# Kernel tuning notes

Hardware: AMD Instinct MI355X
Metric: run time of the kernel (lower is better)

The kernel has to match this reference:

```python
import math
import jax, jax.numpy as jnp
import numpy as np


def setup_inputs() -> dict:
    key = jax.random.key(0)
    k1, k2 = jax.random.split(key)
    N, C, K = 1024, 4096, 16384
    x = jax.random.normal(k1, (N, C), dtype=jnp.float32)
    # xavier_normal for (C, K): std = sqrt(2/(C+K))
    w_std = math.sqrt(2.0 / (C + K))
    weights = jax.random.normal(k2, (C, K), dtype=jnp.float32) * w_std
    std = jnp.float32(10.0)
    return {"x": x, "weights": weights, "std": std}


def reference(x, weights, std):
    # x: (N, C); weights: (C, K)
    N, C = x.shape
    K = weights.shape[1]
    side = int(math.sqrt(K))

    # Squared distances ||w_k - x_n||^2 via expansion (same math as
    # norm(weights[None] - x[..., None], dim=1)**2, without the (N,C,K) tensor)
    x2 = jnp.sum(x * x, axis=1, keepdims=True)            # (N, 1)
    w2 = jnp.sum(weights * weights, axis=0)[None, :]       # (1, K)
    xw = jnp.einsum('nc,ck->nk', x, weights)               # (N, K) GEMM
    norms2 = jnp.maximum(x2 + w2 - 2.0 * xw, 0.0)          # (N, K)

    # Best matching unit (detached in original)
    bmu = jnp.argmin(norms2, axis=-1)                      # (N,) int

    # 2D radial basis over the side x side grid, centered at BMU
    row = (bmu // side).astype(jnp.float32)
    col = (bmu % side).astype(jnp.float32)
    t = jnp.arange(side, dtype=jnp.float32)
    gi, gj = jnp.meshgrid(t, t, indexing='ij')
    grid = jnp.stack([gi.reshape(-1), gj.reshape(-1)], axis=-1)  # (K, 2)
    pt = jnp.stack([row, col], axis=-1)[:, None, :]              # (N, 1, 2)
    d2 = jnp.sum((grid[None] - pt) ** 2, axis=-1)                # (N, K)
    phi = jnp.exp(-0.5 * d2 / (std ** 2))
    phi = phi / jnp.sum(phi, axis=-1, keepdims=True)

    return norms2 * phi
```

## Files before the change

### kernel.cpp

```cpp
#include <hip/hip_runtime.h>
#include <stdint.h>

#define NROWS 1024
#define CDIM  4096
#define KDIM  16384
#define SIDE  128

typedef __attribute__((ext_vector_type(8))) short short8;
typedef __attribute__((ext_vector_type(4))) float f32x4;

static __device__ __forceinline__ unsigned short f2bf(float f) {
  unsigned u = __float_as_uint(f);
  u += 0x7fffu + ((u >> 16) & 1u);
  return (unsigned short)(u >> 16);
}
static __device__ __forceinline__ float bf2f(unsigned short h) {
  return __uint_as_float(((unsigned)h) << 16);
}

#define GLOAD_LDS16(g, l)                                                     \
  __builtin_amdgcn_global_load_lds(                                           \
      (const __attribute__((address_space(1))) void*)(g),                     \
      (__attribute__((address_space(3))) void*)(l), 16, 0, 0)

#define SWZ(o) ((o) ^ (((o) >> 3) & 0x70))

__global__ void k_zero(float* __restrict__ w2) {
  w2[blockIdx.x * 256 + threadIdx.x] = 0.f;
}

__global__ __launch_bounds__(256) void k_wconv(const float* __restrict__ w,
                                               unsigned short* __restrict__ whT,
                                               unsigned short* __restrict__ wlT,
                                               float* __restrict__ w2) {
  __shared__ float T[64][65];
  const int k0 = blockIdx.x * 64, c0 = blockIdx.y * 64;
  const int t = threadIdx.x;
#pragma unroll
  for (int i = 0; i < 4; i++) {
    int e = i * 1024 + t * 4;
    int cr = e >> 6, kc = e & 63;
    float4 v = *(const float4*)(w + (size_t)(c0 + cr) * KDIM + k0 + kc);
    T[cr][kc] = v.x; T[cr][kc + 1] = v.y; T[cr][kc + 2] = v.z; T[cr][kc + 3] = v.w;
  }
  __syncthreads();
#pragma unroll
  for (int i = 0; i < 4; i++) {
    int e = i * 1024 + t * 4;
    int kr = e >> 6, cc = e & 63;
    ushort4 hv, lv;
    float f0 = T[cc + 0][kr], f1 = T[cc + 1][kr];
    float f2 = T[cc + 2][kr], f3 = T[cc + 3][kr];
    hv.x = f2bf(f0); lv.x = f2bf(f0 - bf2f(hv.x));
    hv.y = f2bf(f1); lv.y = f2bf(f1 - bf2f(hv.y));
    hv.z = f2bf(f2); lv.z = f2bf(f2 - bf2f(hv.z));
    hv.w = f2bf(f3); lv.w = f2bf(f3 - bf2f(hv.w));
    size_t off = (size_t)(k0 + kr) * CDIM + c0 + cc;
    *(ushort4*)(whT + off) = hv;
    *(ushort4*)(wlT + off) = lv;
    float s = f0 * f0 + f1 * f1 + f2 * f2 + f3 * f3;
#pragma unroll
    for (int off2 = 8; off2 > 0; off2 >>= 1) s += __shfl_down(s, off2);
    if ((t & 15) == 0) atomicAdd(&w2[k0 + kr], s);
  }
}

__global__ __launch_bounds__(256) void k_xconv(const float* __restrict__ x,
                                               unsigned short* __restrict__ xh) {
  size_t i = ((size_t)blockIdx.x * 256 + threadIdx.x) * 4;
  float4 v = *(const float4*)(x + i);
  ushort4 hv;
  hv.x = f2bf(v.x); hv.y = f2bf(v.y); hv.z = f2bf(v.z); hv.w = f2bf(v.w);
  *(ushort4*)(xh + i) = hv;
}

__global__ void k_x2(const float* __restrict__ x, float* __restrict__ x2) {
  const int n = blockIdx.x, l = threadIdx.x;
  const float* row = x + (size_t)n * CDIM;
  float s = 0.f;
#pragma unroll 4
  for (int i = 0; i < 16; i++) {
    float4 v = *(const float4*)(row + (i * 64 + l) * 4);
    s += v.x * v.x + v.y * v.y + v.z * v.z + v.w * v.w;
  }
#pragma unroll
  for (int off = 32; off > 0; off >>= 1) s += __shfl_down(s, off);
  if (l == 0) x2[n] = s;
}

__global__ __launch_bounds__(512, 2) void k_gemm(
    const unsigned short* __restrict__ xh,
    const unsigned short* __restrict__ whT,
    const float* __restrict__ x2, const float* __restrict__ w2,
    float* __restrict__ out) {
  __shared__ alignas(128) char smem[49152];
  char* const Ah = smem;
  char* const Bh = smem + 32768;
  const int t = threadIdx.x;
  const int b = blockIdx.x;
  const int wg = (b & 7) * 64 + (b >> 3);
  const int m0 = (wg & 3) * 256, n0 = (wg >> 2) * 128;
  const int lane = t & 63, wid = t >> 6;
  const int wr = (wid >> 1) * 64;
  const int wc = (wid & 1) * 64;

  int rowA[4], cbA[4];
  uint32_t loffA[4];
#pragma unroll
  for (int i = 0; i < 4; i++) {
    int o_lin = (i * 512 + t) * 16;
    int o_log = SWZ(o_lin);
    rowA[i] = o_log >> 7;
    cbA[i] = (o_log & 127) >> 1;
    loffA[i] = i * 8192 + wid * 1024;
  }
  int rowB[2], cbB[2];
  uint32_t loffB[2];
#pragma unroll
  for (int i = 0; i < 2; i++) {
    int o_lin = (i * 512 + t) * 16;
    int o_log = SWZ(o_lin);
    rowB[i] = o_log >> 7;
    cbB[i] = (o_log & 127) >> 1;
    loffB[i] = i * 8192 + wid * 1024;
  }

  f32x4 acc[4][4];
#pragma unroll
  for (int m = 0; m < 4; m++)
#pragma unroll
    for (int n = 0; n < 4; n++) acc[m][n] = (f32x4){0.f, 0.f, 0.f, 0.f};

  const int rlo = lane & 15;
  const int kgb = (lane >> 4) * 16;

  for (int c0 = 0; c0 < CDIM; c0 += 64) {
#pragma unroll
    for (int i = 0; i < 4; i++) {
      size_t ga = (size_t)(m0 + rowA[i]) * CDIM + c0 + cbA[i];
      GLOAD_LDS16(xh + ga, Ah + loffA[i]);
    }
#pragma unroll
    for (int i = 0; i < 2; i++) {
      size_t gb = (size_t)(n0 + rowB[i]) * CDIM + c0 + cbB[i];
      GLOAD_LDS16(whT + gb, Bh + loffB[i]);
    }
    __syncthreads();

#pragma unroll
    for (int h = 0; h < 2; h++) {
      const int cby = h * 64 + kgb;
      short8 b_f[4];
#pragma unroll
      for (int n = 0; n < 4; n++)
        b_f[n] = *(const short8*)(Bh + SWZ((wc + n * 16 + rlo) * 128 + cby));
#pragma unroll
      for (int m = 0; m < 4; m++) {
        short8 ah = *(const short8*)(Ah + SWZ((wr + m * 16 + rlo) * 128 + cby));
#pragma unroll
        for (int n = 0; n < 4; n++)
          acc[m][n] = __builtin_amdgcn_mfma_f32_16x16x32_bf16(ah, b_f[n], acc[m][n], 0, 0, 0);
      }
    }
    __syncthreads();
  }

  float w2v[4];
#pragma unroll
  for (int n = 0; n < 4; n++) w2v[n] = w2[n0 + wc + n * 16 + rlo];
#pragma unroll
  for (int m = 0; m < 4; m++) {
#pragma unroll
    for (int j = 0; j < 4; j++) {
      int row = m0 + wr + m * 16 + (lane >> 4) * 4 + j;
      float xr = x2[row];
      float* orow = out + (size_t)row * KDIM;
#pragma unroll
      for (int n = 0; n < 4; n++) {
        int col = n0 + wc + n * 16 + rlo;
        float v = xr + w2v[n] - 2.0f * acc[m][n][j];
        orow[col] = v < 0.f ? 0.f : v;
      }
    }
  }
}

__global__ __launch_bounds__(256) void k_fb(const float* __restrict__ x,
                                            const float* __restrict__ w,
                                            float* __restrict__ out) {
  __shared__ float xs[16][65];
  __shared__ float wsm[16][65];
  const int t = threadIdx.x;
  const int n0 = blockIdx.x * 64, k0 = blockIdx.y * 64;
  const int tx = t & 15, ty = t >> 4;
  float acc[4][4];
#pragma unroll
  for (int a = 0; a < 4; a++)
#pragma unroll
    for (int b = 0; b < 4; b++) acc[a][b] = 0.f;
  for (int c0 = 0; c0 < CDIM; c0 += 16) {
#pragma unroll
    for (int i = 0; i < 4; i++) {
      int e = i * 256 + t;
      int nl = e >> 4, cl = e & 15;
      xs[cl][nl] = x[(size_t)(n0 + nl) * CDIM + c0 + cl];
    }
#pragma unroll
    for (int i = 0; i < 4; i++) {
      int e = i * 256 + t;
      int cl = e >> 6, kl = e & 63;
      wsm[cl][kl] = w[(size_t)(c0 + cl) * KDIM + k0 + kl];
    }
    __syncthreads();
#pragma unroll
    for (int c = 0; c < 16; c++)
#pragma unroll
      for (int a = 0; a < 4; a++) {
        float xa = xs[c][ty * 4 + a];
#pragma unroll
        for (int b = 0; b < 4; b++) {
          float d = wsm[c][tx * 4 + b] - xa;
          acc[a][b] += d * d;
        }
      }
    __syncthreads();
  }
#pragma unroll
  for (int a = 0; a < 4; a++)
#pragma unroll
    for (int b = 0; b < 4; b++)
      out[(size_t)(n0 + ty * 4 + a) * KDIM + k0 + tx * 4 + b] = acc[a][b];
}

__global__ __launch_bounds__(256) void k_row(
    float* __restrict__ out, const float* __restrict__ stdp,
    const float* __restrict__ x, const unsigned short* __restrict__ whT,
    const unsigned short* __restrict__ wlT, const float* __restrict__ w2) {
  const int n = blockIdx.x, t = threadIdx.x;
  __shared__ alignas(16) float er[SIDE];
  __shared__ alignas(16) float ec[SIDE];
  __shared__ float rv[4];
  __shared__ float s_red[4];
  __shared__ int cand[128];
  __shared__ int s_ncand;
  __shared__ int s_bmu;
  __shared__ float s_inv;
  float* row = out + (size_t)n * KDIM;

  float bv = 3.4e38f;
#pragma unroll 4
  for (int i = 0; i < 16; i++) {
    float4 v = *(const float4*)(row + (t + i * 256) * 4);
    bv = fminf(fminf(fminf(bv, v.x), fminf(v.y, v.z)), v.w);
  }
#pragma unroll
  for (int off = 32; off > 0; off >>= 1) bv = fminf(bv, __shfl_down(bv, off));
  if ((t & 63) == 0) rv[t >> 6] = bv;
  if (t == 0) s_ncand = 0;
  __syncthreads();
  const float thr = fminf(fminf(rv[0], rv[1]), fminf(rv[2], rv[3])) + 0.05f;

#pragma unroll 4
  for (int i = 0; i < 16; i++) {
    int k = (t + i * 256) * 4;
    float4 v = *(const float4*)(row + k);
    if (v.x <= thr) { int j = atomicAdd(&s_ncand, 1); if (j < 128) cand[j] = k; }
    if (v.y <= thr) { int j = atomicAdd(&s_ncand, 1); if (j < 128) cand[j] = k + 1; }
    if (v.z <= thr) { int j = atomicAdd(&s_ncand, 1); if (j < 128) cand[j] = k + 2; }
    if (v.w <= thr) { int j = atomicAdd(&s_ncand, 1); if (j < 128) cand[j] = k + 3; }
  }
  __syncthreads();
  int nc = s_ncand < 128 ? s_ncand : 128;

  float best = 3.4e38f;
  int bestk = 0x7fffffff;
  const float* xr = x + (size_t)n * CDIM;
  for (int j = 0; j < nc; j++) {
    const int k = cand[j];
    const unsigned short* wh = whT + (size_t)k * CDIM;
    const unsigned short* wl = wlT + (size_t)k * CDIM;
    float s = 0.f;
#pragma unroll
    for (int ii = 0; ii < 2; ii++) {
      int c = (ii * 256 + t) * 8;
      short8 h8 = *(const short8*)(wh + c);
      short8 l8 = *(const short8*)(wl + c);
      float4 xa = *(const float4*)(xr + c);
      float4 xb = *(const float4*)(xr + c + 4);
      s += xa.x * (bf2f((unsigned short)h8[0]) + bf2f((unsigned short)l8[0]));
      s += xa.y * (bf2f((unsigned short)h8[1]) + bf2f((unsigned short)l8[1]));
      s += xa.z * (bf2f((unsigned short)h8[2]) + bf2f((unsigned short)l8[2]));
      s += xa.w * (bf2f((unsigned short)h8[3]) + bf2f((unsigned short)l8[3]));
      s += xb.x * (bf2f((unsigned short)h8[4]) + bf2f((unsigned short)l8[4]));
      s += xb.y * (bf2f((unsigned short)h8[5]) + bf2f((unsigned short)l8[5]));
      s += xb.z * (bf2f((unsigned short)h8[6]) + bf2f((unsigned short)l8[6]));
      s += xb.w * (bf2f((unsigned short)h8[7]) + bf2f((unsigned short)l8[7]));
    }
#pragma unroll
    for (int off = 32; off > 0; off >>= 1) s += __shfl_down(s, off);
    if ((t & 63) == 0) s_red[t >> 6] = s;
    __syncthreads();
    if (t == 0) {
      float dot = s_red[0] + s_red[1] + s_red[2] + s_red[3];
      float sc = w2[k] - 2.0f * dot;
      if (sc < best || (sc == best && k < bestk)) { best = sc; bestk = k; }
    }
    __syncthreads();
  }
  if (t == 0) s_bmu = bestk;
  __syncthreads();

  const int bmu = s_bmu;
  const float sd = stdp[0];
  const float inv2s2 = -0.5f / (sd * sd);
  const float rr = (float)(bmu >> 7), ccol = (float)(bmu & 127);
  if (t < 128) {
    float d = (float)t - rr;
    er[t] = expf(d * d * inv2s2);
  } else {
    int j = t - 128;
    float d = (float)j - ccol;
    ec[j] = expf(d * d * inv2s2);
  }
  __syncthreads();
  if (t == 0) {
    float Sr = 0.f, Sc = 0.f;
    for (int i = 0; i < SIDE; i++) { Sr += er[i]; Sc += ec[i]; }
    s_inv = 1.0f / (Sr * Sc);
  }
  __syncthreads();
  const float inv = s_inv;
#pragma unroll 4
  for (int i = 0; i < 16; i++) {
    int k = (t + i * 256) * 4;
    float4 v = *(const float4*)(row + k);
    float e_r = er[k >> 7] * inv;
    const float4 e4 = *(const float4*)(&ec[k & 127]);
    v.x *= e_r * e4.x;
    v.y *= e_r * e4.y;
    v.z *= e_r * e4.z;
    v.w *= e_r * e4.w;
    *(float4*)(row + k) = v;
  }
}

__global__ __launch_bounds__(256) void k_row_fb(float* __restrict__ out,
                                                const float* __restrict__ stdp) {
  const int n = blockIdx.x, t = threadIdx.x;
  __shared__ alignas(16) float er[SIDE];
  __shared__ alignas(16) float ec[SIDE];
  __shared__ float rv[4];
  __shared__ int ri[4];
  __shared__ float s_inv;
  __shared__ int s_bmu;
  float* row = out + (size_t)n * KDIM;

  float bv = 3.4e38f;
  int bi = 0;
#pragma unroll 4
  for (int i = 0; i < 16; i++) {
    int k = (t + i * 256) * 4;
    float4 v = *(const float4*)(row + k);
    if (v.x < bv) { bv = v.x; bi = k; }
    if (v.y < bv) { bv = v.y; bi = k + 1; }
    if (v.z < bv) { bv = v.z; bi = k + 2; }
    if (v.w < bv) { bv = v.w; bi = k + 3; }
  }
#pragma unroll
  for (int off = 32; off > 0; off >>= 1) {
    float ov = __shfl_down(bv, off);
    int oi = __shfl_down(bi, off);
    if (ov < bv || (ov == bv && oi < bi)) { bv = ov; bi = oi; }
  }
  if ((t & 63) == 0) { rv[t >> 6] = bv; ri[t >> 6] = bi; }
  __syncthreads();
  if (t == 0) {
    for (int i = 1; i < 4; i++)
      if (rv[i] < bv || (rv[i] == bv && ri[i] < bi)) { bv = rv[i]; bi = ri[i]; }
    s_bmu = bi;
  }
  __syncthreads();
  const int bmu = s_bmu;
  const float sd = stdp[0];
  const float inv2s2 = -0.5f / (sd * sd);
  const float rr = (float)(bmu >> 7), ccol = (float)(bmu & 127);
  if (t < 128) {
    float d = (float)t - rr;
    er[t] = expf(d * d * inv2s2);
  } else {
    int j = t - 128;
    float d = (float)j - ccol;
    ec[j] = expf(d * d * inv2s2);
  }
  __syncthreads();
  if (t == 0) {
    float Sr = 0.f, Sc = 0.f;
    for (int i = 0; i < SIDE; i++) { Sr += er[i]; Sc += ec[i]; }
    s_inv = 1.0f / (Sr * Sc);
  }
  __syncthreads();
  const float inv = s_inv;
#pragma unroll 4
  for (int i = 0; i < 16; i++) {
    int k = (t + i * 256) * 4;
    float4 v = *(const float4*)(row + k);
    float e_r = er[k >> 7] * inv;
    const float4 e4 = *(const float4*)(&ec[k & 127]);
    v.x *= e_r * e4.x;
    v.y *= e_r * e4.y;
    v.z *= e_r * e4.z;
    v.w *= e_r * e4.w;
    *(float4*)(row + k) = v;
  }
}

extern "C" void kernel_launch(void* const* d_in, const int* in_sizes, int n_in,
                              void* d_out, int out_size, void* d_ws, size_t ws_size,
                              hipStream_t stream) {
  (void)in_sizes; (void)n_in; (void)out_size;
  const float* x = (const float*)d_in[0];
  const float* w = (const float*)d_in[1];
  const float* stdp = (const float*)d_in[2];
  float* out = (float*)d_out;

  const size_t sz_wT = (size_t)KDIM * CDIM * sizeof(unsigned short);
  const size_t sz_x  = (size_t)NROWS * CDIM * sizeof(unsigned short);
  const size_t need = 2 * sz_wT + sz_x + (size_t)NROWS * 4 + (size_t)KDIM * 4;

  if (ws_size >= need) {
    char* p = (char*)d_ws;
    unsigned short* whT = (unsigned short*)p; p += sz_wT;
    unsigned short* wlT = (unsigned short*)p; p += sz_wT;
    unsigned short* xh  = (unsigned short*)p; p += sz_x;
    float* x2 = (float*)p; p += (size_t)NROWS * 4;
    float* w2 = (float*)p;

    k_zero<<<KDIM / 256, 256, 0, stream>>>(w2);
    k_wconv<<<dim3(KDIM / 64, CDIM / 64), 256, 0, stream>>>(w, whT, wlT, w2);
    k_xconv<<<(NROWS * CDIM) / 1024, 256, 0, stream>>>(x, xh);
    k_x2<<<NROWS, 64, 0, stream>>>(x, x2);
    k_gemm<<<512, 512, 0, stream>>>(xh, whT, x2, w2, out);
    k_row<<<NROWS, 256, 0, stream>>>(out, stdp, x, whT, wlT, w2);
  } else {
    k_fb<<<dim3(NROWS / 64, KDIM / 64), 256, 0, stream>>>(x, w, out);
    k_row_fb<<<NROWS, 256, 0, stream>>>(out, stdp);
  }
}
```

Measured before the change: 307.8 us.

## Double-buffer GEMM LDS tiles and enlarge block tile to 256x256

The bf16 GEMM kernel moves to a 256x256 output tile per workgroup, with each wave computing 128x64, and halves the grid to 256 blocks. The next K-tile is loaded into a second 64KB LDS buffer while the current one is computed, using explicit vmcnt waits and raw barriers in place of the blocking load-then-sync loop. MFMA sections are given raised wave priority. It needs 128KB of dynamic LDS, which gives one block per CU and doubles the accumulator registers. With only 256 blocks the grid may underfill the GPU's CUs.

New measurement: 293.2 us. 1.05x faster.

```diff
diff --git a/kernel.cpp b/kernel.cpp
--- a/kernel.cpp
+++ b/kernel.cpp
@@ -93,91 +93,102 @@
     const unsigned short* __restrict__ whT,
     const float* __restrict__ x2, const float* __restrict__ w2,
     float* __restrict__ out) {
-  __shared__ alignas(128) char smem[49152];
-  char* const Ah = smem;
-  char* const Bh = smem + 32768;
+  extern __shared__ char smem[];
   const int t = threadIdx.x;
   const int b = blockIdx.x;
-  const int wg = (b & 7) * 64 + (b >> 3);
-  const int m0 = (wg & 3) * 256, n0 = (wg >> 2) * 128;
+  const int L = (b & 7) * 32 + (b >> 3);
+  const int m0 = (L & 3) * 256, n0 = (L >> 2) * 256;
   const int lane = t & 63, wid = t >> 6;
-  const int wr = (wid >> 1) * 64;
-  const int wc = (wid & 1) * 64;
-
-  int rowA[4], cbA[4];
-  uint32_t loffA[4];
+  const int wrow = (wid >> 2) * 128;
+  const int wcol = (wid & 3) * 64;
+
+  int rowS[4], cbS[4];
+  uint32_t loffS[4];
 #pragma unroll
   for (int i = 0; i < 4; i++) {
     int o_lin = (i * 512 + t) * 16;
     int o_log = SWZ(o_lin);
-    rowA[i] = o_log >> 7;
-    cbA[i] = (o_log & 127) >> 1;
-    loffA[i] = i * 8192 + wid * 1024;
-  }
-  int rowB[2], cbB[2];
-  uint32_t loffB[2];
-#pragma unroll
-  for (int i = 0; i < 2; i++) {
-    int o_lin = (i * 512 + t) * 16;
-    int o_log = SWZ(o_lin);
-    rowB[i] = o_log >> 7;
-    cbB[i] = (o_log & 127) >> 1;
-    loffB[i] = i * 8192 + wid * 1024;
-  }
-
-  f32x4 acc[4][4];
-#pragma unroll
-  for (int m = 0; m < 4; m++)
+    rowS[i] = o_log >> 7;
+    cbS[i] = (o_log & 127) >> 1;
+    loffS[i] = i * 8192 + wid * 1024;
+  }
+
+  f32x4 acc[8][4];
+#pragma unroll
+  for (int m = 0; m < 8; m++)
 #pragma unroll
     for (int n = 0; n < 4; n++) acc[m][n] = (f32x4){0.f, 0.f, 0.f, 0.f};
 
   const int rlo = lane & 15;
   const int kgb = (lane >> 4) * 16;
 
-  for (int c0 = 0; c0 < CDIM; c0 += 64) {
-#pragma unroll
-    for (int i = 0; i < 4; i++) {
-      size_t ga = (size_t)(m0 + rowA[i]) * CDIM + c0 + cbA[i];
-      GLOAD_LDS16(xh + ga, Ah + loffA[i]);
-    }
-#pragma unroll
-    for (int i = 0; i < 2; i++) {
-      size_t gb = (size_t)(n0 + rowB[i]) * CDIM + c0 + cbB[i];
-      GLOAD_LDS16(whT + gb, Bh + loffB[i]);
-    }
-    __syncthreads();
-
-#pragma unroll
-    for (int h = 0; h < 2; h++) {
-      const int cby = h * 64 + kgb;
-      short8 b_f[4];
-#pragma unroll
-      for (int n = 0; n < 4; n++)
-        b_f[n] = *(const short8*)(Bh + SWZ((wc + n * 16 + rlo) * 128 + cby));
-#pragma unroll
-      for (int m = 0; m < 4; m++) {
-        short8 ah = *(const short8*)(Ah + SWZ((wr + m * 16 + rlo) * 128 + cby));
-#pragma unroll
-        for (int n = 0; n < 4; n++)
-          acc[m][n] = __builtin_amdgcn_mfma_f32_16x16x32_bf16(ah, b_f[n], acc[m][n], 0, 0, 0);
+#define STAGE_TILE(tt, d)                                                     \
+  {                                                                           \
+    const int c0s = (tt) * 64;                                                \
+    char* const dst = smem + (d) * 65536;                                     \
+    _Pragma("unroll")                                                         \
+    for (int i = 0; i < 4; i++) {                                             \
+      size_t ga = (size_t)(m0 + rowS[i]) * CDIM + c0s + cbS[i];               \
+      GLOAD_LDS16(xh + ga, dst + loffS[i]);                                   \
+    }                                                                         \
+    _Pragma("unroll")                                                         \
+    for (int i = 0; i < 4; i++) {                                             \
+      size_t gb = (size_t)(n0 + rowS[i]) * CDIM + c0s + cbS[i];               \
+      GLOAD_LDS16(whT + gb, dst + 32768 + loffS[i]);                          \
+    }                                                                         \
+  }
+
+  STAGE_TILE(0, 0);
+
+  for (int tl = 0; tl < 64; ++tl) {
+    const int cur = tl & 1;
+    if (tl < 63) {
+      STAGE_TILE(tl + 1, cur ^ 1);
+      asm volatile("s_waitcnt vmcnt(8)" ::: "memory");
+    } else {
+      asm volatile("s_waitcnt vmcnt(0)" ::: "memory");
+    }
+    asm volatile("s_barrier" ::: "memory");
+
+    const char* const Ab = smem + cur * 65536;
+    const char* const Bb = Ab + 32768;
+    short8 b_f[4][2];
+#pragma unroll
+    for (int n = 0; n < 4; n++)
+#pragma unroll
+      for (int ks = 0; ks < 2; ks++)
+        b_f[n][ks] = *(const short8*)(Bb + SWZ((wcol + n * 16 + rlo) * 128 + ks * 64 + kgb));
+    __builtin_amdgcn_s_setprio(1);
+#pragma unroll
+    for (int m = 0; m < 8; m++) {
+      const char* ar = Ab + (wrow + m * 16 + rlo) * 128;
+      short8 a0 = *(const short8*)(Ab + SWZ((wrow + m * 16 + rlo) * 128 + kgb));
+      short8 a1 = *(const short8*)(Ab + SWZ((wrow + m * 16 + rlo) * 128 + 64 + kgb));
+      (void)ar;
+#pragma unroll
+      for (int n = 0; n < 4; n++) {
+        acc[m][n] = __builtin_amdgcn_mfma_f32_16x16x32_bf16(a0, b_f[n][0], acc[m][n], 0, 0, 0);
+        acc[m][n] = __builtin_amdgcn_mfma_f32_16x16x32_bf16(a1, b_f[n][1], acc[m][n], 0, 0, 0);
       }
     }
-    __syncthreads();
-  }
+    __builtin_amdgcn_s_setprio(0);
+    asm volatile("s_barrier" ::: "memory");
+  }
+#undef STAGE_TILE
 
   float w2v[4];
 #pragma unroll
-  for (int n = 0; n < 4; n++) w2v[n] = w2[n0 + wc + n * 16 + rlo];
-#pragma unroll
-  for (int m = 0; m < 4; m++) {
+  for (int n = 0; n < 4; n++) w2v[n] = w2[n0 + wcol + n * 16 + rlo];
+#pragma unroll
+  for (int m = 0; m < 8; m++) {
 #pragma unroll
     for (int j = 0; j < 4; j++) {
-      int row = m0 + wr + m * 16 + (lane >> 4) * 4 + j;
+      int row = m0 + wrow + m * 16 + (lane >> 4) * 4 + j;
       float xr = x2[row];
       float* orow = out + (size_t)row * KDIM;
 #pragma unroll
       for (int n = 0; n < 4; n++) {
-        int col = n0 + wc + n * 16 + rlo;
+        int col = n0 + wcol + n * 16 + rlo;
         float v = xr + w2v[n] - 2.0f * acc[m][n][j];
         orow[col] = v < 0.f ? 0.f : v;
       }
@@ -435,11 +446,17 @@
     float* x2 = (float*)p; p += (size_t)NROWS * 4;
     float* w2 = (float*)p;
 
+    static int lds_ok = -1;
+    if (lds_ok < 0)
+      lds_ok = (int)hipFuncSetAttribute((const void*)k_gemm,
+                                        hipFuncAttributeMaxDynamicSharedMemorySize,
+                                        131072);
+
     k_zero<<<KDIM / 256, 256, 0, stream>>>(w2);
     k_wconv<<<dim3(KDIM / 64, CDIM / 64), 256, 0, stream>>>(w, whT, wlT, w2);
     k_xconv<<<(NROWS * CDIM) / 1024, 256, 0, stream>>>(x, xh);
     k_x2<<<NROWS, 64, 0, stream>>>(x, x2);
-    k_gemm<<<512, 512, 0, stream>>>(xh, whT, x2, w2, out);
+    k_gemm<<<256, 512, 131072, stream>>>(xh, whT, x2, w2, out);
     k_row<<<NROWS, 256, 0, stream>>>(out, stdp, x, whT, wlT, w2);
   } else {
     k_fb<<<dim3(NROWS / 64, KDIM / 64), 256, 0, stream>>>(x, w, out);
```
